# Performance work log

Measured on AMD Instinct MI355X. Metric: run time of the kernel, lower is better.

Reference implementation:

```python
import jax, jax.numpy as jnp
import numpy as np

N = 100_000   # nodes
E = 1_600_000 # edges (avg degree 16)
D0, D1, D2 = 128, 64, 64


def _linp(key, n_out, n_in):
    kw, kb = jax.random.split(key)
    s = 1.0 / np.sqrt(n_in)
    W = jax.random.uniform(kw, (n_out, n_in), jnp.float32, -s, s)
    b = jax.random.uniform(kb, (n_out,), jnp.float32, -s, s)
    return W, b


def setup_inputs() -> dict:
    key = jax.random.key(0)
    ks = jax.random.split(key, 9)
    h = jax.random.normal(ks[0], (N, D0), jnp.float32)
    # guarantee every row has at least one edge (avoids empty-row softmax / 0-std NaNs)
    rows = jnp.concatenate([jnp.arange(N, dtype=jnp.int32),
                            jax.random.randint(ks[1], (E - N,), 0, N, jnp.int32)])
    cols = jax.random.randint(ks[2], (E,), 0, N, jnp.int32)
    edge_index = jnp.stack([rows, cols])  # [2, E], row = softmax segment
    W11, b11 = _linp(ks[3], D1, D0)
    W12, b12 = _linp(ks[4], 1, D1)
    W13, b13 = _linp(ks[5], D1, D0)
    W21, b21 = _linp(ks[6], D2, D1)
    W22, b22 = _linp(ks[7], 1, D2)
    W23, b23 = _linp(ks[8], D2, D1)
    return dict(h=h, edge_index=edge_index,
                W11=W11, b11=b11, W12=W12, b12=b12, W13=W13, b13=b13,
                W21=W21, b21=b21, W22=W22, b22=b22, W23=W23, b23=b23)


def reference(h, edge_index, W11, b11, W12, b12, W13, b13,
              W21, b21, W22, b22, W23, b23):
    src, dst = edge_index[0], edge_index[1]

    def gat_layer(x, Wa, ba, We, be, Wv, bv):
        a = jnp.tanh(x @ Wa.T + ba)                       # [N, d] node scores (l11/l21)
        e = jnp.tanh((a[src] + a[dst]) @ We.T + be)[:, 0] # [E] per-edge logit (l12/l22)
        # per-row (segment) softmax over src = row index
        m = jax.ops.segment_max(e, src, num_segments=N)
        ex = jnp.exp(e - m[src])
        denom = jax.ops.segment_sum(ex, src, num_segments=N)
        att = ex / denom[src]                             # [E]
        v = jnp.tanh(x @ Wv.T + bv)                       # [N, d] values (l13/l23)
        out = jax.ops.segment_sum(att[:, None] * v[dst], src, num_segments=N)  # sparse mm
        return out / jnp.std(out, -1, keepdims=True, ddof=1)  # torch.std is unbiased

    h = gat_layer(h, W11, b11, W12, b12, W13, b13)
    h = gat_layer(h, W21, b21, W22, b22, W23, b23)
    return h
```

## Files before the change

### kernel.cpp

```cpp
#include <hip/hip_runtime.h>


#define WS_ALIGN 256
#define BIN_SHIFT 7
#define BIN_NODES 128
#define BIN_CAP 2560
#define MAX_BINS 1024
#define EPB 4096

typedef __attribute__((ext_vector_type(8))) short short8;
typedef __attribute__((ext_vector_type(4))) float f32x4;

__device__ __forceinline__ float wave_sum(float x) {
#pragma unroll
  for (int m = 32; m > 0; m >>= 1) x += __shfl_xor(x, m, 64);
  return x;
}

__device__ __forceinline__ float fast_tanh(float x) {
  x = fminf(15.f, fmaxf(-15.f, x));
  float e = __expf(2.f * x);
  return (e - 1.f) * __builtin_amdgcn_rcpf(e + 1.f);
}

__device__ __forceinline__ unsigned short f32_to_bf16_rne(float f) {
  unsigned u = __float_as_uint(f);
  unsigned r = u + 0x7fffu + ((u >> 16) & 1u);
  return (unsigned short)(r >> 16);
}

__device__ __forceinline__ float bf16_to_f32(unsigned short b) {
  return __uint_as_float(((unsigned)b) << 16);
}

__global__ void k_init_cursor(int* __restrict__ cursor, int nb) {
  int i = blockIdx.x * 256 + threadIdx.x;
  if (i < nb) cursor[i] = i * BIN_CAP;
}

__global__ __launch_bounds__(256) void k_bin(const int* __restrict__ src,
                                             const int* __restrict__ dst,
                                             int* __restrict__ cursor,
                                             int* __restrict__ binned, int E, int nb) {
  __shared__ int ssrc[EPB];
  __shared__ int sdst[EPB];
  __shared__ int hist[MAX_BINS];
  __shared__ int base[MAX_BINS];
  int t = threadIdx.x;
  for (int i = t; i < nb; i += 256) hist[i] = 0;
  __syncthreads();
  int e0 = blockIdx.x * EPB;
  for (int i = t; i < EPB; i += 256) {
    int e = e0 + i;
    int sv = -1, dv = 0;
    if (e < E) {
      sv = src[e];
      dv = dst[e];
      atomicAdd(&hist[sv >> BIN_SHIFT], 1);
    }
    ssrc[i] = sv;
    sdst[i] = dv;
  }
  __syncthreads();
  for (int b = t; b < nb; b += 256) {
    int c = hist[b];
    base[b] = c ? atomicAdd(&cursor[b], c) : 0;
    hist[b] = 0;
  }
  __syncthreads();
  for (int i = t; i < EPB; i += 256) {
    int sv = ssrc[i];
    if (sv >= 0) {
      int b = sv >> BIN_SHIFT;
      int r = atomicAdd(&hist[b], 1);
      int pos = base[b] + r;
      if (pos < (b + 1) * BIN_CAP)
        binned[pos] = (sdst[i] << BIN_SHIFT) | (sv & (BIN_NODES - 1));
    }
  }
}

__global__ __launch_bounds__(256) void k_sort_bin(int* __restrict__ binned,
                                                  const int* __restrict__ cursor,
                                                  int* __restrict__ rs,
                                                  int* __restrict__ re, int n) {
  __shared__ int ents[BIN_CAP];
  __shared__ int sorted[BIN_CAP];
  __shared__ int hist[BIN_NODES];
  __shared__ int scan[BIN_NODES];
  __shared__ int cur[BIN_NODES];
  int bin = blockIdx.x;
  int t = threadIdx.x;
  int nbase = bin << BIN_SHIFT;
  int cnt = cursor[bin] - bin * BIN_CAP;
  if (cnt > BIN_CAP) cnt = BIN_CAP;
  if (t < BIN_NODES) hist[t] = 0;
  __syncthreads();
  int* bp = binned + (size_t)bin * BIN_CAP;
  for (int i = t; i < cnt; i += 256) {
    int pk = bp[i];
    ents[i] = pk;
    atomicAdd(&hist[pk & (BIN_NODES - 1)], 1);
  }
  __syncthreads();
  if (t < BIN_NODES) scan[t] = hist[t];
  __syncthreads();
  for (int off = 1; off < BIN_NODES; off <<= 1) {
    int add = (t < BIN_NODES && t >= off) ? scan[t - off] : 0;
    __syncthreads();
    if (t < BIN_NODES) scan[t] += add;
    __syncthreads();
  }
  if (t < BIN_NODES) {
    int ex = scan[t] - hist[t];
    cur[t] = ex;
    int node = nbase + t;
    if (node < n) {
      rs[node] = bin * BIN_CAP + ex;
      re[node] = bin * BIN_CAP + ex + hist[t];
    }
  }
  __syncthreads();
  for (int i = t; i < cnt; i += 256) {
    int pk = ents[i];
    int pos = atomicAdd(&cur[pk & (BIN_NODES - 1)], 1);
    sorted[pos] = pk >> BIN_SHIFT;
  }
  __syncthreads();
  for (int i = t; i < cnt; i += 256) bp[i] = sorted[i];
}

__global__ void k_prepw(const float* __restrict__ Wa, const float* __restrict__ Wv,
                        short* __restrict__ Wh, short* __restrict__ Wl, int K) {
  int i = blockIdx.x * 256 + threadIdx.x;
  if (i >= 128 * K) return;
  int KBLK = K / 32;
  int j = i & 7;
  int c = (i >> 3) & 15;
  int q = (i >> 7) & 3;
  int r = i >> 9;
  int nt = r / KBLK, kb = r - nt * KBLK;
  int row = nt * 16 + c;
  int col = kb * 32 + q * 8 + j;
  float f = (row < 64) ? Wa[row * K + col] : Wv[(row - 64) * K + col];
  unsigned u = __float_as_uint(f);
  float hf = __uint_as_float(u & 0xffff0000u);
  Wh[i] = (short)(u >> 16);
  Wl[i] = (short)(__float_as_uint(f - hf) >> 16);
}

template <int K>
__global__ __launch_bounds__(256) void k_node(
    const float* __restrict__ x, const short* __restrict__ Wh,
    const short* __restrict__ Wl, const float* __restrict__ ba,
    const float* __restrict__ we, const float* __restrict__ bv,
    unsigned short* __restrict__ v_out, float* __restrict__ s_out, int n) {
  constexpr int KBLK = K / 32;
  constexpr int KP = K + 4;
  __shared__ float sx[64 * KP];
  int t = threadIdx.x;
  int l = t & 63;
  int w = t >> 6;
  int q = l >> 4, c = l & 15;
  int node0b = blockIdx.x * 64;

  {
    const float4* xg = (const float4*)(x + (size_t)node0b * K);
    constexpr int R4 = K / 4;
#pragma unroll
    for (int it = 0; it < 64 * R4 / 256; it++) {
      int i = it * 256 + t;
      int r = i / R4, k4 = i - r * R4;
      float4 val = (node0b + r < n) ? xg[i] : (float4){0.f, 0.f, 0.f, 0.f};
      *(float4*)&sx[r * KP + k4 * 4] = val;
    }
  }
  __syncthreads();

  int node0w = node0b + w * 16;
  if (node0w >= n) return;

  const short8* WhF = (const short8*)Wh;
  const short8* WlF = (const short8*)Wl;

  f32x4 acc[8];
#pragma unroll
  for (int i = 0; i < 8; i++) acc[i] = (f32x4){0.f, 0.f, 0.f, 0.f};

  const float* xl = sx + (w * 16 + c) * KP;

#pragma unroll 1
  for (int kb = 0; kb < KBLK; kb++) {
    float4 x0 = *(const float4*)&xl[kb * 32 + q * 8];
    float4 x1 = *(const float4*)&xl[kb * 32 + q * 8 + 4];
    float xv[8] = {x0.x, x0.y, x0.z, x0.w, x1.x, x1.y, x1.z, x1.w};
    short8 ah, al;
#pragma unroll
    for (int j = 0; j < 8; j++) {
      unsigned u = __float_as_uint(xv[j]);
      ah[j] = (short)(u >> 16);
      float hf = __uint_as_float(u & 0xffff0000u);
      al[j] = (short)(__float_as_uint(xv[j] - hf) >> 16);
    }
#pragma unroll
    for (int nt = 0; nt < 8; nt++) {
      short8 wh = WhF[(size_t)(nt * KBLK + kb) * 64 + l];
      short8 wl = WlF[(size_t)(nt * KBLK + kb) * 64 + l];
      acc[nt] = __builtin_amdgcn_mfma_f32_16x16x32_bf16(ah, wh, acc[nt], 0, 0, 0);
      acc[nt] = __builtin_amdgcn_mfma_f32_16x16x32_bf16(ah, wl, acc[nt], 0, 0, 0);
      acc[nt] = __builtin_amdgcn_mfma_f32_16x16x32_bf16(al, wh, acc[nt], 0, 0, 0);
    }
  }

  float p[4] = {0.f, 0.f, 0.f, 0.f};
#pragma unroll
  for (int nt = 0; nt < 4; nt++) {
    int o = nt * 16 + c;
    float bav = ba[o], wev = we[o];
#pragma unroll
    for (int r = 0; r < 4; r++) p[r] += fast_tanh(acc[nt][r] + bav) * wev;
  }
#pragma unroll
  for (int mm = 1; mm < 16; mm <<= 1) {
#pragma unroll
    for (int r = 0; r < 4; r++) p[r] += __shfl_xor(p[r], mm, 64);
  }
  if (c == 0) {
#pragma unroll
    for (int r = 0; r < 4; r++) {
      int node = node0w + q * 4 + r;
      if (node < n) s_out[node] = p[r];
    }
  }
#pragma unroll
  for (int nt = 4; nt < 8; nt++) {
    int o = (nt - 4) * 16 + c;
    float bvv = bv[o];
#pragma unroll
    for (int r = 0; r < 4; r++) {
      int node = node0w + q * 4 + r;
      if (node < n)
        v_out[(size_t)node * 64 + o] = f32_to_bf16_rne(fast_tanh(acc[nt][r] + bvv));
    }
  }
}

__global__ __launch_bounds__(256) void k_aggr(const int* __restrict__ rs,
                                              const int* __restrict__ re,
                                              const int* __restrict__ col,
                                              const float* __restrict__ s,
                                              const float* __restrict__ be_p,
                                              const unsigned short* __restrict__ v,
                                              float* __restrict__ out, int n) {
  int gw = (int)((blockIdx.x * 256 + threadIdx.x) >> 6);
  int l = threadIdx.x & 63;
  if (gw >= n) return;
  int e0 = rs[gw], e1 = re[gw];
  float srow = s[gw];
  float be = be_p[0];
  float acc = 0.f, denom = 0.f;

  for (int base = e0; base < e1; base += 64) {
    int m = e1 - base;
    if (m > 64) m = 64;
    int c = 0;
    float w = 0.f;
    if (l < m) {
      c = col[base + l];
      w = __expf(fast_tanh(srow + s[c] + be));
    }
    denom += wave_sum(w);

    int j = 0;
    for (; j + 8 <= m; j += 8) {
      int c0 = __shfl(c, j), c1 = __shfl(c, j + 1), c2 = __shfl(c, j + 2), c3 = __shfl(c, j + 3);
      int c4 = __shfl(c, j + 4), c5 = __shfl(c, j + 5), c6 = __shfl(c, j + 6), c7 = __shfl(c, j + 7);
      float w0 = __shfl(w, j), w1 = __shfl(w, j + 1), w2 = __shfl(w, j + 2), w3 = __shfl(w, j + 3);
      float w4 = __shfl(w, j + 4), w5 = __shfl(w, j + 5), w6 = __shfl(w, j + 6), w7 = __shfl(w, j + 7);
      float v0 = bf16_to_f32(v[(size_t)c0 * 64 + l]);
      float v1 = bf16_to_f32(v[(size_t)c1 * 64 + l]);
      float v2 = bf16_to_f32(v[(size_t)c2 * 64 + l]);
      float v3 = bf16_to_f32(v[(size_t)c3 * 64 + l]);
      float v4 = bf16_to_f32(v[(size_t)c4 * 64 + l]);
      float v5 = bf16_to_f32(v[(size_t)c5 * 64 + l]);
      float v6 = bf16_to_f32(v[(size_t)c6 * 64 + l]);
      float v7 = bf16_to_f32(v[(size_t)c7 * 64 + l]);
      acc = fmaf(w0, v0, acc);
      acc = fmaf(w1, v1, acc);
      acc = fmaf(w2, v2, acc);
      acc = fmaf(w3, v3, acc);
      acc = fmaf(w4, v4, acc);
      acc = fmaf(w5, v5, acc);
      acc = fmaf(w6, v6, acc);
      acc = fmaf(w7, v7, acc);
    }
    for (; j + 4 <= m; j += 4) {
      int c0 = __shfl(c, j), c1 = __shfl(c, j + 1), c2 = __shfl(c, j + 2), c3 = __shfl(c, j + 3);
      float w0 = __shfl(w, j), w1 = __shfl(w, j + 1), w2 = __shfl(w, j + 2), w3 = __shfl(w, j + 3);
      float v0 = bf16_to_f32(v[(size_t)c0 * 64 + l]);
      float v1 = bf16_to_f32(v[(size_t)c1 * 64 + l]);
      float v2 = bf16_to_f32(v[(size_t)c2 * 64 + l]);
      float v3 = bf16_to_f32(v[(size_t)c3 * 64 + l]);
      acc = fmaf(w0, v0, acc);
      acc = fmaf(w1, v1, acc);
      acc = fmaf(w2, v2, acc);
      acc = fmaf(w3, v3, acc);
    }
    for (; j < m; j++) {
      int cj = __shfl(c, j);
      float wj = __shfl(w, j);
      acc = fmaf(wj, bf16_to_f32(v[(size_t)cj * 64 + l]), acc);
    }
  }

  float o = acc / denom;
  float sum = wave_sum(o);
  float sumsq = wave_sum(o * o);
  float var = (sumsq - sum * sum * (1.0f / 64.f)) * (1.0f / 63.f);
  out[(size_t)gw * 64 + l] = o / sqrtf(var);
}

extern "C" void kernel_launch(void* const* d_in, const int* in_sizes, int n_in,
                              void* d_out, int out_size, void* d_ws, size_t ws_size,
                              hipStream_t stream) {
  const float* h = (const float*)d_in[0];
  const int* ei = (const int*)d_in[1];
  const float* W11 = (const float*)d_in[2];
  const float* b11 = (const float*)d_in[3];
  const float* W12 = (const float*)d_in[4];
  const float* b12 = (const float*)d_in[5];
  const float* W13 = (const float*)d_in[6];
  const float* b13 = (const float*)d_in[7];
  const float* W21 = (const float*)d_in[8];
  const float* b21 = (const float*)d_in[9];
  const float* W22 = (const float*)d_in[10];
  const float* b22 = (const float*)d_in[11];
  const float* W23 = (const float*)d_in[12];
  const float* b23 = (const float*)d_in[13];

  const int N = in_sizes[0] / 128;
  const int E = in_sizes[1] / 2;
  const int* src = ei;
  const int* dst = ei + E;
  const int NB = (N + BIN_NODES - 1) >> BIN_SHIFT;

  char* p = (char*)d_ws;
  auto alloc = [&](size_t bytes) -> void* {
    void* r = (void*)p;
    p += (bytes + WS_ALIGN - 1) / WS_ALIGN * WS_ALIGN;
    return r;
  };
  int* cursor = (int*)alloc((size_t)NB * 4);
  int* binned = (int*)alloc((size_t)NB * BIN_CAP * 4);
  int* rsb = (int*)alloc((size_t)N * 4);
  int* reb = (int*)alloc((size_t)N * 4);
  float* sbuf = (float*)alloc((size_t)N * 4);
  unsigned short* vbuf = (unsigned short*)alloc((size_t)N * 64 * 2);
  float* out1 = (float*)alloc((size_t)N * 64 * 4);
  short* Wh1 = (short*)alloc(128 * 128 * 2);
  short* Wl1 = (short*)alloc(128 * 128 * 2);
  short* Wh2 = (short*)alloc(128 * 64 * 2);
  short* Wl2 = (short*)alloc(128 * 64 * 2);

  k_prepw<<<(128 * 128 + 255) / 256, 256, 0, stream>>>(W11, W13, Wh1, Wl1, 128);
  k_prepw<<<(128 * 64 + 255) / 256, 256, 0, stream>>>(W21, W23, Wh2, Wl2, 64);

  k_init_cursor<<<(NB + 255) / 256, 256, 0, stream>>>(cursor, NB);
  k_bin<<<(E + EPB - 1) / EPB, 256, 0, stream>>>(src, dst, cursor, binned, E, NB);
  k_sort_bin<<<NB, 256, 0, stream>>>(binned, cursor, rsb, reb, N);

  k_node<128><<<(N + 63) / 64, 256, 0, stream>>>(h, Wh1, Wl1, b11, W12, b13, vbuf, sbuf, N);
  k_aggr<<<(N * 64 + 255) / 256, 256, 0, stream>>>(rsb, reb, binned, sbuf, b12, vbuf, out1, N);

  k_node<64><<<(N + 63) / 64, 256, 0, stream>>>(out1, Wh2, Wl2, b21, W22, b23, vbuf, sbuf, N);
  k_aggr<<<(N * 64 + 255) / 256, 256, 0, stream>>>(rsb, reb, binned, sbuf, b22, vbuf, (float*)d_out, N);
}
```

Before: 315.6 us.

## Vectorize aggregation gathers across 4 edges per wave and fuse setup kernels

New measurement: 303.7 us. 3.8% less time.

```diff
diff --git a/kernel.cpp b/kernel.cpp
--- a/kernel.cpp
+++ b/kernel.cpp
@@ -29,13 +29,39 @@
   return (unsigned short)(r >> 16);
 }
 
-__device__ __forceinline__ float bf16_to_f32(unsigned short b) {
-  return __uint_as_float(((unsigned)b) << 16);
-}
-
-__global__ void k_init_cursor(int* __restrict__ cursor, int nb) {
+__device__ __forceinline__ void prepw_one(const float* __restrict__ Wa,
+                                          const float* __restrict__ Wv,
+                                          short* __restrict__ Wh, short* __restrict__ Wl,
+                                          int K, int i) {
+  int KBLK = K / 32;
+  int j = i & 7;
+  int c = (i >> 3) & 15;
+  int q = (i >> 7) & 3;
+  int r = i >> 9;
+  int nt = r / KBLK, kb = r - nt * KBLK;
+  int row = nt * 16 + c;
+  int col = kb * 32 + q * 8 + j;
+  float f = (row < 64) ? Wa[row * K + col] : Wv[(row - 64) * K + col];
+  unsigned u = __float_as_uint(f);
+  float hf = __uint_as_float(u & 0xffff0000u);
+  Wh[i] = (short)(u >> 16);
+  Wl[i] = (short)(__float_as_uint(f - hf) >> 16);
+}
+
+__global__ void k_setup(const float* __restrict__ W11, const float* __restrict__ W13,
+                        short* __restrict__ Wh1, short* __restrict__ Wl1,
+                        const float* __restrict__ W21, const float* __restrict__ W23,
+                        short* __restrict__ Wh2, short* __restrict__ Wl2,
+                        int* __restrict__ cursor, int nb) {
   int i = blockIdx.x * 256 + threadIdx.x;
-  if (i < nb) cursor[i] = i * BIN_CAP;
+  if (i < 16384) {
+    prepw_one(W11, W13, Wh1, Wl1, 128, i);
+  } else if (i < 16384 + 8192) {
+    prepw_one(W21, W23, Wh2, Wl2, 64, i - 16384);
+  } else {
+    int b = i - 24576;
+    if (b < nb) cursor[b] = b * BIN_CAP;
+  }
 }
 
 __global__ __launch_bounds__(256) void k_bin(const int* __restrict__ src,
@@ -130,25 +156,6 @@
   for (int i = t; i < cnt; i += 256) bp[i] = sorted[i];
 }
 
-__global__ void k_prepw(const float* __restrict__ Wa, const float* __restrict__ Wv,
-                        short* __restrict__ Wh, short* __restrict__ Wl, int K) {
-  int i = blockIdx.x * 256 + threadIdx.x;
-  if (i >= 128 * K) return;
-  int KBLK = K / 32;
-  int j = i & 7;
-  int c = (i >> 3) & 15;
-  int q = (i >> 7) & 3;
-  int r = i >> 9;
-  int nt = r / KBLK, kb = r - nt * KBLK;
-  int row = nt * 16 + c;
-  int col = kb * 32 + q * 8 + j;
-  float f = (row < 64) ? Wa[row * K + col] : Wv[(row - 64) * K + col];
-  unsigned u = __float_as_uint(f);
-  float hf = __uint_as_float(u & 0xffff0000u);
-  Wh[i] = (short)(u >> 16);
-  Wl[i] = (short)(__float_as_uint(f - hf) >> 16);
-}
-
 template <int K>
 __global__ __launch_bounds__(256) void k_node(
     const float* __restrict__ x, const short* __restrict__ Wh,
@@ -258,7 +265,10 @@
   int e0 = rs[gw], e1 = re[gw];
   float srow = s[gw];
   float be = be_p[0];
-  float acc = 0.f, denom = 0.f;
+  int es = l >> 4;
+  int g = l & 15;
+  float a0 = 0.f, a1 = 0.f, a2 = 0.f, a3 = 0.f;
+  float denom = 0.f;
 
   for (int base = e0; base < e1; base += 64) {
     int m = e1 - base;
@@ -270,54 +280,36 @@
       w = __expf(fast_tanh(srow + s[c] + be));
     }
     denom += wave_sum(w);
-
-    int j = 0;
-    for (; j + 8 <= m; j += 8) {
-      int c0 = __shfl(c, j), c1 = __shfl(c, j + 1), c2 = __shfl(c, j + 2), c3 = __shfl(c, j + 3);
-      int c4 = __shfl(c, j + 4), c5 = __shfl(c, j + 5), c6 = __shfl(c, j + 6), c7 = __shfl(c, j + 7);
-      float w0 = __shfl(w, j), w1 = __shfl(w, j + 1), w2 = __shfl(w, j + 2), w3 = __shfl(w, j + 3);
-      float w4 = __shfl(w, j + 4), w5 = __shfl(w, j + 5), w6 = __shfl(w, j + 6), w7 = __shfl(w, j + 7);
-      float v0 = bf16_to_f32(v[(size_t)c0 * 64 + l]);
-      float v1 = bf16_to_f32(v[(size_t)c1 * 64 + l]);
-      float v2 = bf16_to_f32(v[(size_t)c2 * 64 + l]);
-      float v3 = bf16_to_f32(v[(size_t)c3 * 64 + l]);
-      float v4 = bf16_to_f32(v[(size_t)c4 * 64 + l]);
-      float v5 = bf16_to_f32(v[(size_t)c5 * 64 + l]);
-      float v6 = bf16_to_f32(v[(size_t)c6 * 64 + l]);
-      float v7 = bf16_to_f32(v[(size_t)c7 * 64 + l]);
-      acc = fmaf(w0, v0, acc);
-      acc = fmaf(w1, v1, acc);
-      acc = fmaf(w2, v2, acc);
-      acc = fmaf(w3, v3, acc);
-      acc = fmaf(w4, v4, acc);
-      acc = fmaf(w5, v5, acc);
-      acc = fmaf(w6, v6, acc);
-      acc = fmaf(w7, v7, acc);
-    }
-    for (; j + 4 <= m; j += 4) {
-      int c0 = __shfl(c, j), c1 = __shfl(c, j + 1), c2 = __shfl(c, j + 2), c3 = __shfl(c, j + 3);
-      float w0 = __shfl(w, j), w1 = __shfl(w, j + 1), w2 = __shfl(w, j + 2), w3 = __shfl(w, j + 3);
-      float v0 = bf16_to_f32(v[(size_t)c0 * 64 + l]);
-      float v1 = bf16_to_f32(v[(size_t)c1 * 64 + l]);
-      float v2 = bf16_to_f32(v[(size_t)c2 * 64 + l]);
-      float v3 = bf16_to_f32(v[(size_t)c3 * 64 + l]);
-      acc = fmaf(w0, v0, acc);
-      acc = fmaf(w1, v1, acc);
-      acc = fmaf(w2, v2, acc);
-      acc = fmaf(w3, v3, acc);
-    }
-    for (; j < m; j++) {
+    int iters = (m + 3) >> 2;
+    for (int it = 0; it < iters; it++) {
+      int j = (it << 2) + es;
       int cj = __shfl(c, j);
       float wj = __shfl(w, j);
-      acc = fmaf(wj, bf16_to_f32(v[(size_t)cj * 64 + l]), acc);
-    }
-  }
-
-  float o = acc / denom;
-  float sum = wave_sum(o);
-  float sumsq = wave_sum(o * o);
-  float var = (sumsq - sum * sum * (1.0f / 64.f)) * (1.0f / 63.f);
-  out[(size_t)gw * 64 + l] = o / sqrtf(var);
+      uint2 pk = *(const uint2*)(v + ((size_t)cj << 6) + (g << 2));
+      a0 = fmaf(wj, __uint_as_float(pk.x << 16), a0);
+      a1 = fmaf(wj, __uint_as_float(pk.x & 0xffff0000u), a1);
+      a2 = fmaf(wj, __uint_as_float(pk.y << 16), a2);
+      a3 = fmaf(wj, __uint_as_float(pk.y & 0xffff0000u), a3);
+    }
+  }
+
+#pragma unroll
+  for (int mm = 16; mm < 64; mm <<= 1) {
+    a0 += __shfl_xor(a0, mm, 64);
+    a1 += __shfl_xor(a1, mm, 64);
+    a2 += __shfl_xor(a2, mm, 64);
+    a3 += __shfl_xor(a3, mm, 64);
+  }
+  float inv = __builtin_amdgcn_rcpf(denom);
+  float o0 = a0 * inv, o1 = a1 * inv, o2 = a2 * inv, o3 = a3 * inv;
+  float ls = wave_sum(o0 + o1 + o2 + o3) * 0.25f;
+  float lq = wave_sum(o0 * o0 + o1 * o1 + o2 * o2 + o3 * o3) * 0.25f;
+  float var = (lq - ls * ls * (1.0f / 64.f)) * (1.0f / 63.f);
+  float isd = __builtin_amdgcn_rsqf(var);
+  if (es == 0) {
+    float4 r = {o0 * isd, o1 * isd, o2 * isd, o3 * isd};
+    *(float4*)&out[(size_t)gw * 64 + (g << 2)] = r;
+  }
 }
 
 extern "C" void kernel_launch(void* const* d_in, const int* in_sizes, int n_in,
@@ -362,10 +354,9 @@
   short* Wh2 = (short*)alloc(128 * 64 * 2);
   short* Wl2 = (short*)alloc(128 * 64 * 2);
 
-  k_prepw<<<(128 * 128 + 255) / 256, 256, 0, stream>>>(W11, W13, Wh1, Wl1, 128);
-  k_prepw<<<(128 * 64 + 255) / 256, 256, 0, stream>>>(W21, W23, Wh2, Wl2, 64);
-
-  k_init_cursor<<<(NB + 255) / 256, 256, 0, stream>>>(cursor, NB);
+  k_setup<<<(24576 + NB + 255) / 256, 256, 0, stream>>>(
+      W11, W13, Wh1, Wl1, W21, W23, Wh2, Wl2, cursor, NB);
+
   k_bin<<<(E + EPB - 1) / EPB, 256, 0, stream>>>(src, dst, cursor, binned, E, NB);
   k_sort_bin<<<NB, 256, 0, stream>>>(binned, cursor, rsb, reb, N);
 
```
